# Optimization experiments

Measured on AMD Instinct MI355X. Metric: run time of the kernel, lower is better.

The kernel has to match this reference:

```python
import jax, jax.numpy as jnp
import numpy as np

N_NODES = 50000


def gcn_conv(x, src, dst, W, b, n_nodes):
    """PyG GCNConv: self-loops + symmetric normalization D^-1/2 (A+I) D^-1/2 X W + b."""
    loop = jnp.arange(n_nodes, dtype=src.dtype)
    s = jnp.concatenate([src, loop])
    d = jnp.concatenate([dst, loop])
    deg = jax.ops.segment_sum(jnp.ones_like(d, dtype=x.dtype), d, num_segments=n_nodes)
    dinv = jnp.where(deg > 0, jax.lax.rsqrt(deg), 0.0)
    norm = dinv[s] * dinv[d]  # (E+N,)
    h = x @ W  # (N, out)
    msg = h[s] * norm[:, None]
    return jax.ops.segment_sum(msg, d, num_segments=n_nodes) + b


def setup_inputs() -> dict:
    key = jax.random.key(0)
    ks = jax.random.split(key, 16)
    N, S, D = N_NODES, 20, 128
    E = 1_600_000
    PH, PO, GH, GO = 64, 128, 128, 32

    def lin(k, fan_in, fan_out):
        bound = 1.0 / np.sqrt(fan_in)
        kw, kb = jax.random.split(k)
        W = jax.random.uniform(kw, (fan_in, fan_out), jnp.float32, -bound, bound)
        b = jax.random.uniform(kb, (fan_out,), jnp.float32, -bound, bound)
        return W, b

    W_embed, b_embed = lin(ks[0], D, PH)
    W_attn, b_attn = lin(ks[1], PH, 1)
    W_out, b_out = lin(ks[2], PH, PO)
    W1, b1 = lin(ks[3], PO, GH)
    W2, b2 = lin(ks[4], GH, GO)
    Wm1, bm1 = lin(ks[5], GO, 64)
    Wm2, bm2 = lin(ks[6], 64, 1)

    return {
        "set_features": jax.random.normal(ks[7], (N, S, D), jnp.float32),
        "set_mask": jnp.ones((N, S), jnp.int32),
        "edge_index": jax.random.randint(ks[8], (2, E), 0, N, jnp.int32),
        "query_idx": jax.random.randint(ks[9], (4096,), 0, N, jnp.int32),
        "W_embed": W_embed, "b_embed": b_embed,
        "W_attn": W_attn, "b_attn": b_attn,
        "W_out": W_out, "b_out": b_out,
        "W1": W1, "b1": b1, "W2": W2, "b2": b2,
        "Wm1": Wm1, "bm1": bm1, "Wm2": Wm2, "bm2": bm2,
    }


def reference(set_features, set_mask, edge_index, query_idx,
              W_embed, b_embed, W_attn, b_attn, W_out, b_out,
              W1, b1, W2, b2, Wm1, bm1, Wm2, bm2):
    n_nodes = set_features.shape[0]
    # Attention pooling over each node's set: (N, S, D) -> (N, PO)
    z = jax.nn.relu(set_features @ W_embed + b_embed)          # (N, S, PH)
    scores = (z @ W_attn)[..., 0] + b_attn[0]                  # (N, S)
    scores = jnp.where(set_mask == 0, -jnp.inf, scores)
    attn = jax.nn.softmax(scores, axis=1)                      # (N, S)
    pooled = jnp.einsum('nsh,ns->nh', z, attn) @ W_out + b_out  # (N, PO)

    src, dst = edge_index[0], edge_index[1]
    x = jax.nn.relu(gcn_conv(pooled, src, dst, W1, b1, n_nodes))
    x = jax.nn.relu(gcn_conv(x, src, dst, W2, b2, n_nodes))

    q = x[query_idx]                                            # (B, GO)
    logits = (jax.nn.relu(q @ Wm1 + bm1) @ Wm2 + bm2)[..., 0]   # (B,)
    return logits
```

## Files before the change

kernel.cpp:

```cpp
#include <hip/hip_runtime.h>
#include <math.h>

#define RFL(x) __builtin_amdgcn_readfirstlane(x)
#define RL(x, l) __int_as_float(__builtin_amdgcn_readlane(__float_as_int(x), (l)))

typedef __attribute__((ext_vector_type(8))) short bf16x8;
typedef __attribute__((ext_vector_type(4))) float f32x4;

__device__ inline unsigned short bf16_rne(float f) {
  unsigned u = __float_as_uint(f);
  u += 0x7FFFu + ((u >> 16) & 1u);
  return (unsigned short)(u >> 16);
}


__global__ __launch_bounds__(256) void k_zero(int* p, int n) {
  int t = blockIdx.x * 256 + threadIdx.x;
  if (t < n) p[t] = 0;
}

__global__ __launch_bounds__(256) void k_count(const int* __restrict__ dst, int* cnt, int E) {
  int stride = gridDim.x * blockDim.x;
  for (int e = blockIdx.x * blockDim.x + threadIdx.x; e < E; e += stride)
    atomicAdd(&cnt[dst[e]], 1);
}


__global__ __launch_bounds__(256) void k_scan1(const int* __restrict__ cnt, int* __restrict__ row,
                                               int* __restrict__ partial, int N) {
  __shared__ int sm[256];
  int t = threadIdx.x, g = blockIdx.x * 256 + t;
  int v = (g < N) ? cnt[g] : 0;
  sm[t] = v;
  __syncthreads();
#pragma unroll
  for (int off = 1; off < 256; off <<= 1) {
    int x = 0;
    if (t >= off) x = sm[t - off];
    __syncthreads();
    if (t >= off) sm[t] += x;
    __syncthreads();
  }
  if (g < N) row[g] = sm[t] - v;
  if (t == 255) partial[blockIdx.x] = sm[255];
}

__global__ __launch_bounds__(256) void k_scan2(int* __restrict__ partial, int P) {
  __shared__ int sm[256];
  int t = threadIdx.x;
  int carry = 0;
  for (int base = 0; base < P; base += 256) {
    int idx = base + t;
    int v = (idx < P) ? partial[idx] : 0;
    sm[t] = v;
    __syncthreads();
#pragma unroll
    for (int off = 1; off < 256; off <<= 1) {
      int x = 0;
      if (t >= off) x = sm[t - off];
      __syncthreads();
      if (t >= off) sm[t] += x;
      __syncthreads();
    }
    if (idx < P) partial[idx] = carry + sm[t] - v;
    int tot = sm[255];
    __syncthreads();
    carry += tot;
  }
}

__global__ __launch_bounds__(256) void k_scan3(int* __restrict__ row, const int* __restrict__ partial,
                                               int* __restrict__ cursor, const int* __restrict__ cnt,
                                               float* __restrict__ dinv, int N) {
  int g = blockIdx.x * 256 + threadIdx.x;
  if (g < N) {
    int v = row[g] + partial[blockIdx.x];
    row[g] = v;
    cursor[g] = v;
    dinv[g] = rsqrtf((float)cnt[g] + 1.0f);
  }
}


__global__ __launch_bounds__(256) void k_edge_fill(const int* __restrict__ src, const int* __restrict__ dst,
                                                   int* __restrict__ cursor, int* __restrict__ esrc, int E) {
  int stride = gridDim.x * blockDim.x;
  for (int e = blockIdx.x * blockDim.x + threadIdx.x; e < E; e += stride) {
    int s = src[e], d = dst[e];
    int pos = atomicAdd(&cursor[d], 1);
    esrc[pos] = s;
  }
}


__global__ __launch_bounds__(256) void k_wc(const float* __restrict__ Wout, const float* __restrict__ bout,
                                            const float* __restrict__ W1, float* __restrict__ Wc,
                                            float* __restrict__ bc) {
  int t = blockIdx.x * 256 + threadIdx.x;
  if (t >= 65 * 128) return;
  int h = t >> 7, o = t & 127;
  const float* row = (h < 64) ? (Wout + h * 128) : bout;
  float a = 0.f;
  for (int d = 0; d < 128; ++d) a += row[d] * W1[d * 128 + o];
  if (h < 64) Wc[h * 128 + o] = a;
  else bc[o] = a;
}


__global__ __launch_bounds__(256, 3) void k_pool(const float* __restrict__ X, const int* __restrict__ mask,
                                                 const float* __restrict__ WE, const float* __restrict__ bE,
                                                 const float* __restrict__ WA, const float* __restrict__ bA,
                                                 const float* __restrict__ dinv, float* __restrict__ pzp, int N) {
  __shared__ __align__(16) unsigned short Xh[80][136];
  __shared__ __align__(16) unsigned short Xl[80][136];
  __shared__ float scorep[80][4];
  __shared__ float sco[80];
  __shared__ float wgtA[80];
  float* zt = (float*)&Xh[0][0];

  const int t = threadIdx.x;
  const int lane = t & 63;
  const int wv = t >> 6;
  const int cb = wv * 16;
  const int l16 = lane & 15;
  const int lg = lane >> 4;

  const long long totRows = (long long)N * 20;
  const int numTiles = (N + 3) / 4;

  const int r0 = t >> 5;
  const int kq4 = (t & 31) * 4;

  bf16x8 bh[4], bl[4];
#pragma unroll
  for (int kk = 0; kk < 4; ++kk) {
    union { bf16x8 v; unsigned short s[8]; } uh, ul;
#pragma unroll
    for (int i = 0; i < 8; ++i) {
      int k = kk * 32 + lg * 8 + i;
      float w = WE[k * 64 + cb + l16];
      unsigned short h = bf16_rne(w);
      uh.s[i] = h;
      ul.s[i] = bf16_rne(w - __uint_as_float((unsigned)h << 16));
    }
    bh[kk] = uh.v;
    bl[kk] = ul.v;
  }
  const float bEv = bE[cb + l16];
  const float WAv = WA[cb + l16];
  const float bAv = bA[0];
  const float NEG = -3.0e38f;

  int tile = blockIdx.x;
  if (tile >= numTiles) return;

  float4 xv[10];
#pragma unroll
  for (int q = 0; q < 10; ++q) {
    long long rr = (long long)tile * 80 + r0 + q * 8;
    if (rr >= totRows) rr = totRows - 1;
    xv[q] = *(const float4*)(X + rr * 128 + kq4);
  }
  int mkcur = 1;
  {
    long long mi = (long long)tile * 80 + t;
    if (t < 80) mkcur = (mi < totRows) ? mask[mi] : 0;
  }

  while (true) {
#pragma unroll
    for (int q = 0; q < 10; ++q) {
      const int r = r0 + q * 8;
      const float4 v = xv[q];
      unsigned short h0 = bf16_rne(v.x), h1 = bf16_rne(v.y), h2 = bf16_rne(v.z), h3 = bf16_rne(v.w);
      float f0 = __uint_as_float((unsigned)h0 << 16);
      float f1 = __uint_as_float((unsigned)h1 << 16);
      float f2 = __uint_as_float((unsigned)h2 << 16);
      float f3 = __uint_as_float((unsigned)h3 << 16);
      *(ushort4*)&Xh[r][kq4] = make_ushort4(h0, h1, h2, h3);
      *(ushort4*)&Xl[r][kq4] = make_ushort4(bf16_rne(v.x - f0), bf16_rne(v.y - f1),
                                            bf16_rne(v.z - f2), bf16_rne(v.w - f3));
    }
    __syncthreads();

    const int nextTile = tile + gridDim.x;
    const bool hasNext = nextTile < numTiles;
    float4 xn[10];
    int mknext = 1;
    {
      const long long nb = (long long)(hasNext ? nextTile : tile) * 80;
#pragma unroll
      for (int q = 0; q < 10; ++q) {
        long long rr = nb + r0 + q * 8;
        if (rr >= totRows) rr = totRows - 1;
        xn[q] = *(const float4*)(X + rr * 128 + kq4);
      }
      long long mi = nb + t;
      if (t < 80) mknext = (mi < totRows) ? mask[mi] : 0;
    }

    f32x4 acc[5];
#pragma unroll
    for (int rt = 0; rt < 5; ++rt) acc[rt] = (f32x4){0.f, 0.f, 0.f, 0.f};
#pragma unroll
    for (int rt = 0; rt < 5; ++rt) {
      const int rl = rt * 16 + l16;
#pragma unroll
      for (int kk = 0; kk < 4; ++kk) {
        const int ko = kk * 32 + lg * 8;
        bf16x8 ah = *(const bf16x8*)&Xh[rl][ko];
        bf16x8 al = *(const bf16x8*)&Xl[rl][ko];
        acc[rt] = __builtin_amdgcn_mfma_f32_16x16x32_bf16(ah, bh[kk], acc[rt], 0, 0, 0);
        acc[rt] = __builtin_amdgcn_mfma_f32_16x16x32_bf16(ah, bl[kk], acc[rt], 0, 0, 0);
        acc[rt] = __builtin_amdgcn_mfma_f32_16x16x32_bf16(al, bh[kk], acc[rt], 0, 0, 0);
      }
    }

#pragma unroll
    for (int rt = 0; rt < 5; ++rt) {
#pragma unroll
      for (int j = 0; j < 4; ++j) {
        float z = fmaxf(acc[rt][j] + bEv, 0.f);
        acc[rt][j] = z;
        float v = z * WAv;
        v += __shfl_xor(v, 1, 64);
        v += __shfl_xor(v, 2, 64);
        v += __shfl_xor(v, 4, 64);
        v += __shfl_xor(v, 8, 64);
        if (l16 == 0) scorep[rt * 16 + lg * 4 + j][wv] = v;
      }
    }
    __syncthreads();

#pragma unroll
    for (int rt = 0; rt < 5; ++rt) {
#pragma unroll
      for (int j = 0; j < 4; ++j) {
        int row = rt * 16 + lg * 4 + j;
        zt[row * 68 + cb + l16] = acc[rt][j];
      }
    }
    if (t < 80) {
      float4 sp = *(const float4*)scorep[t];
      float sc = sp.x + sp.y + sp.z + sp.w + bAv;
      if (mkcur == 0) sc = NEG;
      sco[t] = sc;
    }
    __syncthreads();

    if (t < 80) {
      const int base = (t / 20) * 20;
      float mx = NEG;
#pragma unroll
      for (int i = 0; i < 20; ++i) mx = fmaxf(mx, sco[base + i]);
      float den = 0.f;
#pragma unroll
      for (int i = 0; i < 20; ++i) den += __expf(sco[base + i] - mx);
      wgtA[t] = __expf(sco[t] - mx) / den;
    }
    __syncthreads();

    {
      int n = t >> 6, col = t & 63;
      long long node = (long long)tile * 4 + n;
      if (node < N) {
        float s = 0.f;
#pragma unroll
        for (int i = 0; i < 20; ++i) s += zt[(n * 20 + i) * 68 + col] * wgtA[n * 20 + i];
        pzp[node * 64 + col] = s * dinv[node];
      }
    }

    if (!hasNext) break;
    __syncthreads();
#pragma unroll
    for (int q = 0; q < 10; ++q) xv[q] = xn[q];
    mkcur = mknext;
    tile = nextTile;
  }
}


__global__ __launch_bounds__(256) void k_gather1(const int* __restrict__ row, const int* __restrict__ cnt,
                                                 const int* __restrict__ esrc, const float* __restrict__ pzp,
                                                 const float* __restrict__ dinv, float* __restrict__ y,
                                                 float* __restrict__ gout, int N) {
  const int lane = threadIdx.x & 63;
  const int node = RFL(blockIdx.x * 4 + (threadIdx.x >> 6));
  if (node >= N) return;
  const int q = lane >> 4, f4 = lane & 15;
  const int rs = RFL(row[node]);
  const int ne = RFL(cnt[node]);
  const float di = dinv[node];
  const float4* __restrict__ hv = (const float4*)pzp;
  float a0 = 0.f, a1 = 0.f, a2 = 0.f, a3 = 0.f, ds = 0.f;
  int j = 0;
  for (; j + 16 <= ne; j += 16) {
    const int b = rs + j + q * 4;
    int s[4];
#pragma unroll
    for (int u = 0; u < 4; ++u) s[u] = esrc[b + u];
    float4 v[4];
#pragma unroll
    for (int u = 0; u < 4; ++u) v[u] = hv[(size_t)s[u] * 16 + f4];
#pragma unroll
    for (int u = 0; u < 4; ++u) {
      a0 += v[u].x; a1 += v[u].y; a2 += v[u].z; a3 += v[u].w;
      ds += dinv[s[u]];
    }
  }
  if (j < ne) {
    const int b = j + q * 4;
    int s[4];
    float m[4];
#pragma unroll
    for (int u = 0; u < 4; ++u) {
      int idx = b + u;
      int c = (idx < ne) ? idx : (ne - 1);
      s[u] = esrc[rs + c];
      m[u] = (idx < ne) ? 1.f : 0.f;
    }
    float4 v[4];
#pragma unroll
    for (int u = 0; u < 4; ++u) v[u] = hv[(size_t)s[u] * 16 + f4];
#pragma unroll
    for (int u = 0; u < 4; ++u) {
      a0 += v[u].x * m[u]; a1 += v[u].y * m[u]; a2 += v[u].z * m[u]; a3 += v[u].w * m[u];
      ds += dinv[s[u]] * m[u];
    }
  }
  a0 += __shfl_xor(a0, 16, 64); a0 += __shfl_xor(a0, 32, 64);
  a1 += __shfl_xor(a1, 16, 64); a1 += __shfl_xor(a1, 32, 64);
  a2 += __shfl_xor(a2, 16, 64); a2 += __shfl_xor(a2, 32, 64);
  a3 += __shfl_xor(a3, 16, 64); a3 += __shfl_xor(a3, 32, 64);
  ds += __shfl_xor(ds, 16, 64); ds += __shfl_xor(ds, 32, 64);
  if (lane < 16) {
    float4 sv = hv[(size_t)node * 16 + f4];
    float4 o;
    o.x = (a0 + sv.x * di) * di;
    o.y = (a1 + sv.y * di) * di;
    o.z = (a2 + sv.z * di) * di;
    o.w = (a3 + sv.w * di) * di;
    ((float4*)y)[(size_t)node * 16 + f4] = o;
    if (f4 == 0) gout[node] = di * (ds + di * di);
  }
}


__global__ __launch_bounds__(256, 2) void k_gemm1(const float* __restrict__ y, const float* __restrict__ gin,
                                                  const float* __restrict__ Wc, const float* __restrict__ bc,
                                                  float* __restrict__ x1, int N) {
  const int lane = threadIdx.x & 63;
  float w0[64], w1[64];
#pragma unroll
  for (int d = 0; d < 64; ++d) {
    w0[d] = Wc[d * 128 + lane];
    w1[d] = Wc[d * 128 + 64 + lane];
  }
  const float b0 = bc[lane], b1v = bc[64 + lane];
  const int nw = (gridDim.x * blockDim.x) >> 6;
  const int w_id = (blockIdx.x * blockDim.x + threadIdx.x) >> 6;
  for (int r = w_id; r < N; r += nw) {
    const float xv = y[(size_t)r * 64 + lane];
    const float gr = gin[r];
    const int xi = __float_as_int(xv);
    float p0 = 0.f, p1 = 0.f, p2 = 0.f, p3 = 0.f;
#pragma unroll
    for (int d0 = 0; d0 < 64; d0 += 2) {
      float a0 = RL((float&)xi, d0);
      float a1 = RL((float&)xi, d0 + 1);
      p0 += a0 * w0[d0];
      p1 += a0 * w1[d0];
      p2 += a1 * w0[d0 + 1];
      p3 += a1 * w1[d0 + 1];
    }
    size_t o = (size_t)r * 128 + lane;
    x1[o] = p0 + p2 + gr * b0;
    x1[o + 64] = p1 + p3 + gr * b1v;
  }
}


__global__ __launch_bounds__(256, 2) void k_gemm2(const float* __restrict__ x1, const float* __restrict__ b1,
                                                  const float* __restrict__ W2, const float* __restrict__ dinv,
                                                  float* __restrict__ h2p, int N) {
  const int lane = threadIdx.x & 63;
  const int col = lane & 31;
  float w[128];
#pragma unroll
  for (int d = 0; d < 128; ++d) w[d] = W2[d * 32 + col];
  const float bb0 = b1[lane], bb1 = b1[64 + lane];
  const int nw = (gridDim.x * blockDim.x) >> 6;
  const int w_id = (blockIdx.x * blockDim.x + threadIdx.x) >> 6;
  for (int r = w_id; r < N; r += nw) {
    float rx0 = fmaxf(x1[(size_t)r * 128 + lane] + bb0, 0.f);
    float rx1 = fmaxf(x1[(size_t)r * 128 + 64 + lane] + bb1, 0.f);
    const int xi0 = __float_as_int(rx0), xi1 = __float_as_int(rx1);
    float p0 = 0.f, p1 = 0.f, p2 = 0.f, p3 = 0.f;
#pragma unroll
    for (int d0 = 0; d0 < 64; d0 += 2) {
      float a0 = RL((float&)xi0, d0);
      float a1 = RL((float&)xi0, d0 + 1);
      float c0 = RL((float&)xi1, d0);
      float c1 = RL((float&)xi1, d0 + 1);
      p0 += a0 * w[d0];
      p1 += a1 * w[d0 + 1];
      p2 += c0 * w[64 + d0];
      p3 += c1 * w[64 + d0 + 1];
    }
    if (lane < 32) {
      float di = dinv[r];
      h2p[(size_t)r * 32 + col] = ((p0 + p1) + (p2 + p3)) * di;
    }
  }
}


__global__ __launch_bounds__(256) void k_gather2(const int* __restrict__ row, const int* __restrict__ cnt,
                                                 const int* __restrict__ esrc, const float* __restrict__ h2p,
                                                 const float* __restrict__ dinv, float* __restrict__ x2, int N) {
  const int lane = threadIdx.x & 63;
  const int node = RFL(blockIdx.x * 4 + (threadIdx.x >> 6));
  if (node >= N) return;
  const int q = lane >> 3, f4 = lane & 7;
  const int rs = RFL(row[node]);
  const int ne = RFL(cnt[node]);
  const float di = dinv[node];
  const float4* __restrict__ hv = (const float4*)h2p;
  float a0 = 0.f, a1 = 0.f, a2 = 0.f, a3 = 0.f;
  int j = 0;
  for (; j + 32 <= ne; j += 32) {
    const int b = rs + j + q * 4;
    int s[4];
#pragma unroll
    for (int u = 0; u < 4; ++u) s[u] = esrc[b + u];
    float4 v[4];
#pragma unroll
    for (int u = 0; u < 4; ++u) v[u] = hv[(size_t)s[u] * 8 + f4];
#pragma unroll
    for (int u = 0; u < 4; ++u) {
      a0 += v[u].x; a1 += v[u].y; a2 += v[u].z; a3 += v[u].w;
    }
  }
  if (j < ne) {
    const int b = j + q * 4;
    int s[4];
    float m[4];
#pragma unroll
    for (int u = 0; u < 4; ++u) {
      int idx = b + u;
      int c = (idx < ne) ? idx : (ne - 1);
      s[u] = esrc[rs + c];
      m[u] = (idx < ne) ? 1.f : 0.f;
    }
    float4 v[4];
#pragma unroll
    for (int u = 0; u < 4; ++u) v[u] = hv[(size_t)s[u] * 8 + f4];
#pragma unroll
    for (int u = 0; u < 4; ++u) {
      a0 += v[u].x * m[u]; a1 += v[u].y * m[u]; a2 += v[u].z * m[u]; a3 += v[u].w * m[u];
    }
  }
#pragma unroll
  for (int off = 8; off <= 32; off <<= 1) {
    a0 += __shfl_xor(a0, off, 64);
    a1 += __shfl_xor(a1, off, 64);
    a2 += __shfl_xor(a2, off, 64);
    a3 += __shfl_xor(a3, off, 64);
  }
  if (q == 0) {
    float4 sv = hv[(size_t)node * 8 + f4];
    float4 o;
    o.x = (a0 + sv.x * di) * di;
    o.y = (a1 + sv.y * di) * di;
    o.z = (a2 + sv.z * di) * di;
    o.w = (a3 + sv.w * di) * di;
    ((float4*)x2)[(size_t)node * 8 + f4] = o;
  }
}


__global__ __launch_bounds__(256) void k_mlp(const int* __restrict__ qidx, const float* __restrict__ x2,
                                             const float* __restrict__ b2, const float* __restrict__ Wm1,
                                             const float* __restrict__ bm1, const float* __restrict__ Wm2,
                                             const float* __restrict__ bm2, float* __restrict__ out, int B) {
  int t = blockIdx.x * 256 + threadIdx.x;
  if (t >= B) return;
  int n = qidx[t];
  float qv[32];
#pragma unroll
  for (int k = 0; k < 32; ++k) qv[k] = fmaxf(x2[(size_t)n * 32 + k] + b2[k], 0.f);
  float acc = bm2[0];
  for (int j = 0; j < 64; ++j) {
    float h = bm1[j];
#pragma unroll
    for (int k = 0; k < 32; ++k) h += qv[k] * Wm1[k * 64 + j];
    acc += fmaxf(h, 0.f) * Wm2[j];
  }
  out[t] = acc;
}


extern "C" void kernel_launch(void* const* d_in, const int* in_sizes, int n_in,
                              void* d_out, int out_size, void* d_ws, size_t ws_size,
                              hipStream_t stream) {
  const float* X    = (const float*)d_in[0];
  const int*   mask = (const int*)d_in[1];
  const int*   ei   = (const int*)d_in[2];
  const int*   qidx = (const int*)d_in[3];
  const float* WE   = (const float*)d_in[4];
  const float* bE   = (const float*)d_in[5];
  const float* WA   = (const float*)d_in[6];
  const float* bA   = (const float*)d_in[7];
  const float* Wout = (const float*)d_in[8];
  const float* bout = (const float*)d_in[9];
  const float* W1   = (const float*)d_in[10];
  const float* b1   = (const float*)d_in[11];
  const float* W2   = (const float*)d_in[12];
  const float* b2   = (const float*)d_in[13];
  const float* Wm1  = (const float*)d_in[14];
  const float* bm1  = (const float*)d_in[15];
  const float* Wm2  = (const float*)d_in[16];
  const float* bm2  = (const float*)d_in[17];

  const int N = in_sizes[1] / 20;
  const int E = in_sizes[2] / 2;
  const int B = in_sizes[3];
  const int* src  = ei;
  const int* dstp = ei + E;

  const size_t Na = ((size_t)N + 63) & ~(size_t)63;
  const size_t Ea = ((size_t)E + 63) & ~(size_t)63;
  const int P = (N + 255) / 256;
  const size_t Pa = ((size_t)P + 63) & ~(size_t)63;

  float* ws      = (float*)d_ws;
  float* dinv    = ws;
  int*   cnt     = (int*)(dinv + Na);
  int*   rowp    = cnt + Na;
  int*   cursor  = rowp + Na;
  int*   partial = cursor + Na;
  int*   esrc    = partial + Pa;
  float* Wc      = (float*)(esrc + Ea);
  float* bc      = Wc + 8192;
  float* gbuf    = bc + 128;
  float* pzp     = gbuf + Na;
  float* y       = pzp + (size_t)N * 64;
  float* x1      = y + (size_t)N * 64;
  float* h2p     = pzp;
  float* x2      = pzp + (size_t)N * 32;

  const int nb = (N + 255) / 256;
  const int nw4 = (N + 3) / 4;
  const int poolBlocks = ((N + 3) / 4 < 768) ? (N + 3) / 4 : 768;

  k_zero<<<nb, 256, 0, stream>>>(cnt, N);
  k_count<<<1024, 256, 0, stream>>>(dstp, cnt, E);
  k_scan1<<<P, 256, 0, stream>>>(cnt, rowp, partial, N);
  k_scan2<<<1, 256, 0, stream>>>(partial, P);
  k_scan3<<<P, 256, 0, stream>>>(rowp, partial, cursor, cnt, dinv, N);
  k_edge_fill<<<1024, 256, 0, stream>>>(src, dstp, cursor, esrc, E);
  k_wc<<<33, 256, 0, stream>>>(Wout, bout, W1, Wc, bc);
  k_pool<<<poolBlocks, 256, 0, stream>>>(X, mask, WE, bE, WA, bA, dinv, pzp, N);
  k_gather1<<<nw4, 256, 0, stream>>>(rowp, cnt, esrc, pzp, dinv, y, gbuf, N);
  k_gemm1<<<1024, 256, 0, stream>>>(y, gbuf, Wc, bc, x1, N);
  k_gemm2<<<1024, 256, 0, stream>>>(x1, b1, W2, dinv, h2p, N);
  k_gather2<<<nw4, 256, 0, stream>>>(rowp, cnt, esrc, h2p, dinv, x2, N);
  k_mlp<<<(B + 255) / 256, 256, 0, stream>>>(qidx, x2, b2, Wm1, bm1, Wm2, bm2, (float*)d_out, B);
}
```

Before: 510.5 us.

## Compute second GCN aggregation only for queried nodes and fuse the MLP head

The final layer's neighbor gather now runs only for the 4096 query nodes, not all 50000 nodes, and the MLP head is fused into the same kernel. Each wave aggregates one query node, applies bias and ReLU, stages the result in shared memory, then computes the 64-wide hidden layer across lanes with a shuffle reduction. This removes most of the second gather's edge traffic and the x2 round trip through global memory. Duplicate query indices are recomputed rather than shared.

```diff
diff --git a/kernel.cpp b/kernel.cpp
--- a/kernel.cpp
+++ b/kernel.cpp
@@ -416,12 +416,19 @@
 }
 
 
-__global__ __launch_bounds__(256) void k_gather2(const int* __restrict__ row, const int* __restrict__ cnt,
-                                                 const int* __restrict__ esrc, const float* __restrict__ h2p,
-                                                 const float* __restrict__ dinv, float* __restrict__ x2, int N) {
+__global__ __launch_bounds__(256) void k_gmlp(const int* __restrict__ qidx, const int* __restrict__ row,
+                                              const int* __restrict__ cnt, const int* __restrict__ esrc,
+                                              const float* __restrict__ h2p, const float* __restrict__ dinv,
+                                              const float* __restrict__ b2, const float* __restrict__ Wm1,
+                                              const float* __restrict__ bm1, const float* __restrict__ Wm2,
+                                              const float* __restrict__ bm2, float* __restrict__ out, int B) {
+  __shared__ float qs[4][32];
   const int lane = threadIdx.x & 63;
-  const int node = RFL(blockIdx.x * 4 + (threadIdx.x >> 6));
-  if (node >= N) return;
+  const int wv = threadIdx.x >> 6;
+  const int w = blockIdx.x * 4 + wv;
+  const int wc = (w < B) ? w : (B - 1);
+  const int node = RFL(qidx[wc]);
+
   const int q = lane >> 3, f4 = lane & 7;
   const int rs = RFL(row[node]);
   const int ne = RFL(cnt[node]);
@@ -470,34 +477,20 @@
   }
   if (q == 0) {
     float4 sv = hv[(size_t)node * 8 + f4];
-    float4 o;
-    o.x = (a0 + sv.x * di) * di;
-    o.y = (a1 + sv.y * di) * di;
-    o.z = (a2 + sv.z * di) * di;
-    o.w = (a3 + sv.w * di) * di;
-    ((float4*)x2)[(size_t)node * 8 + f4] = o;
-  }
-}
-
-
-__global__ __launch_bounds__(256) void k_mlp(const int* __restrict__ qidx, const float* __restrict__ x2,
-                                             const float* __restrict__ b2, const float* __restrict__ Wm1,
-                                             const float* __restrict__ bm1, const float* __restrict__ Wm2,
-                                             const float* __restrict__ bm2, float* __restrict__ out, int B) {
-  int t = blockIdx.x * 256 + threadIdx.x;
-  if (t >= B) return;
-  int n = qidx[t];
-  float qv[32];
-#pragma unroll
-  for (int k = 0; k < 32; ++k) qv[k] = fmaxf(x2[(size_t)n * 32 + k] + b2[k], 0.f);
-  float acc = bm2[0];
-  for (int j = 0; j < 64; ++j) {
-    float h = bm1[j];
-#pragma unroll
-    for (int k = 0; k < 32; ++k) h += qv[k] * Wm1[k * 64 + j];
-    acc += fmaxf(h, 0.f) * Wm2[j];
-  }
-  out[t] = acc;
+    qs[wv][f4 * 4 + 0] = fmaxf((a0 + sv.x * di) * di + b2[f4 * 4 + 0], 0.f);
+    qs[wv][f4 * 4 + 1] = fmaxf((a1 + sv.y * di) * di + b2[f4 * 4 + 1], 0.f);
+    qs[wv][f4 * 4 + 2] = fmaxf((a2 + sv.z * di) * di + b2[f4 * 4 + 2], 0.f);
+    qs[wv][f4 * 4 + 3] = fmaxf((a3 + sv.w * di) * di + b2[f4 * 4 + 3], 0.f);
+  }
+  __syncthreads();
+
+  float h = bm1[lane];
+#pragma unroll
+  for (int k = 0; k < 32; ++k) h += qs[wv][k] * Wm1[k * 64 + lane];
+  float r = fmaxf(h, 0.f) * Wm2[lane];
+#pragma unroll
+  for (int off = 1; off < 64; off <<= 1) r += __shfl_xor(r, off, 64);
+  if (lane == 0 && w < B) out[w] = r + bm2[0];
 }
 
 
@@ -548,7 +541,6 @@
   float* y       = pzp + (size_t)N * 64;
   float* x1      = y + (size_t)N * 64;
   float* h2p     = pzp;
-  float* x2      = pzp + (size_t)N * 32;
 
   const int nb = (N + 255) / 256;
   const int nw4 = (N + 3) / 4;
@@ -565,6 +557,6 @@
   k_gather1<<<nw4, 256, 0, stream>>>(rowp, cnt, esrc, pzp, dinv, y, gbuf, N);
   k_gemm1<<<1024, 256, 0, stream>>>(y, gbuf, Wc, bc, x1, N);
   k_gemm2<<<1024, 256, 0, stream>>>(x1, b1, W2, dinv, h2p, N);
-  k_gather2<<<nw4, 256, 0, stream>>>(rowp, cnt, esrc, h2p, dinv, x2, N);
-  k_mlp<<<(B + 255) / 256, 256, 0, stream>>>(qidx, x2, b2, Wm1, bm1, Wm2, bm2, (float*)d_out, B);
-}
+  k_gmlp<<<(B + 3) / 4, 256, 0, stream>>>(qidx, rowp, cnt, esrc, h2p, dinv, b2, Wm1, bm1, Wm2, bm2,
+                                          (float*)d_out, B);
+}
```

Measured after the change: 476.2 us. 6.7% less time.
